# Optimization experiments

Hardware: AMD Instinct MI355X
Metric: run time of the kernel (lower is better)

The kernel has to match this reference:

```python
import jax, jax.numpy as jnp
import numpy as np

B, H, S, D = 4, 16, 2048, 64
SCALE = float(D ** 0.5)


def setup_inputs() -> dict:
    key = jax.random.key(0)
    kq, kk, kv = jax.random.split(key, 3)
    q = jax.random.normal(kq, (B, H, S, D), dtype=jnp.float32)
    k = jax.random.normal(kk, (B, H, S, D), dtype=jnp.float32)
    v = jax.random.normal(kv, (B, H, S, D), dtype=jnp.float32)
    return {"q": q, "k": k, "v": v}


def reference(q, k, v):
    # score: (B, H, S, S)
    score = jnp.einsum('bhqd,bhkd->bhqk', q, k) / SCALE
    seq_len = q.shape[-2]
    # causal mask: True above the diagonal (future positions) -> -inf
    mask = jnp.triu(jnp.ones((seq_len, seq_len), dtype=bool), k=1)
    score = jnp.where(mask, -jnp.inf, score)
    attn = jax.nn.softmax(score, axis=-1)
    return jnp.einsum('bhqk,bhkd->bhqd', attn, v)
```

## Files before the change

### kernel.cpp

```cpp
#include <hip/hip_runtime.h>
#include <math.h>

constexpr int S = 2048, D = 64;
constexpr int BH = 64;
constexpr int QTILE = 256;
constexpr int KVB = 64;
constexpr float QSCALE = 0.18033688011112042f;
constexpr float MBIAS = -8.0f;

typedef float f32x4 __attribute__((ext_vector_type(4)));
typedef float f32x16 __attribute__((ext_vector_type(16)));
typedef _Float16 f16x8 __attribute__((ext_vector_type(8)));
typedef unsigned int u32;
typedef unsigned int u32x2 __attribute__((ext_vector_type(2)));
typedef unsigned int u32x4 __attribute__((ext_vector_type(4)));

#define MFMA32(a, b, c) __builtin_amdgcn_mfma_f32_32x32x16_f16((a), (b), (c), 0, 0, 0)

#if __has_builtin(__builtin_amdgcn_exp2f)
#define EXP2(x) __builtin_amdgcn_exp2f(x)
#else
#define EXP2(x) exp2f(x)
#endif

__device__ __forceinline__ u32 pkbits(float a, float b) {
  return __builtin_bit_cast(u32, __builtin_amdgcn_cvt_pkrtz(a, b));
}
__device__ __forceinline__ void plswap(u32& a, u32& b) {
  asm volatile("v_permlane32_swap_b32 %0, %1" : "+v"(a), "+v"(b));
}
__device__ __forceinline__ int swzb(int row) { return ((row & 7) ^ (row >> 3)) << 3; }

#define BARRIER_LGKM()                                          \
  do {                                                          \
    asm volatile("s_waitcnt lgkmcnt(0)" ::: "memory");          \
    __builtin_amdgcn_s_barrier();                               \
    __builtin_amdgcn_sched_barrier(0);                          \
  } while (0)

__device__ __forceinline__ void qk_tile(
    const int ctmax, const int q32, const int hi,
    const _Float16* __restrict__ Kb, const f16x8 (&bq)[4],
    f32x16& st0, f32x16& st1) {
#pragma unroll
  for (int r = 0; r < 16; ++r) { st0[r] = MBIAS; st1[r] = MBIAS; }
  __builtin_amdgcn_s_setprio(1);
#pragma unroll
  for (int t = 0; t < 4; ++t) {
    f16x8 a = *(const f16x8*)&Kb[(q32 << 6) + (swzb(q32) ^ (16 * t + 8 * hi))];
    st0 = MFMA32(a, bq[t], st0);
  }
  if (ctmax) {
    const int row = 32 + q32;
#pragma unroll
    for (int t = 0; t < 4; ++t) {
      f16x8 a = *(const f16x8*)&Kb[(row << 6) + (swzb(row) ^ (16 * t + 8 * hi))];
      st1 = MFMA32(a, bq[t], st1);
    }
  }
  __builtin_amdgcn_s_setprio(0);
}

__device__ __forceinline__ void smpv_tile(
    const int rel, const int ctmax, const int q32, const int hi,
    const _Float16* __restrict__ Vb,
    f32x16& st0, f32x16& st1, f32x16& od0, f32x16& od1, float& l) {
  const bool needmask = (32 * ctmax + 31 > rel);
  if (needmask) {
    const int qrel = rel + q32;
#pragma unroll
    for (int gq = 0; gq < 4; ++gq)
#pragma unroll
      for (int i = 0; i < 4; ++i) {
        if (8 * gq + 4 * hi + i > qrel) st0[4 * gq + i] = -INFINITY;
        if (ctmax && (32 + 8 * gq + 4 * hi + i > qrel)) st1[4 * gq + i] = -INFINITY;
      }
  }

  float ps = 0.f;
#pragma unroll
  for (int r = 0; r < 16; ++r) { const float p = EXP2(st0[r]); st0[r] = p; ps += p; }
  if (ctmax)
#pragma unroll
    for (int r = 0; r < 16; ++r) { const float p = EXP2(st1[r]); st1[r] = p; ps += p; }
  l += ps;

  __builtin_amdgcn_s_setprio(1);
#define PV_CT(stv, CT)                                                          \
  _Pragma("unroll")                                                             \
  for (int t = 0; t < 2; ++t) {                                                 \
    u32 x0 = pkbits(stv[8 * t + 0], stv[8 * t + 1]);                            \
    u32 x1 = pkbits(stv[8 * t + 2], stv[8 * t + 3]);                            \
    u32 y0 = pkbits(stv[8 * t + 4], stv[8 * t + 5]);                            \
    u32 y1 = pkbits(stv[8 * t + 6], stv[8 * t + 7]);                            \
    plswap(x0, y0); plswap(x1, y1);                                             \
    const f16x8 pf = __builtin_bit_cast(f16x8, (u32x4){x0, x1, y0, y1});        \
    const int kcol = (2 * (CT) + t) * 16 + 8 * hi;                              \
    { const f16x8 vf = *(const f16x8*)&Vb[(q32 << 6) + (swzb(q32) ^ kcol)];     \
      od0 = MFMA32(vf, pf, od0); }                                              \
    { const int row = 32 + q32;                                                 \
      const f16x8 vf = *(const f16x8*)&Vb[(row << 6) + (swzb(row) ^ kcol)];     \
      od1 = MFMA32(vf, pf, od1); }                                              \
  }
  PV_CT(st0, 0);
  if (ctmax) { PV_CT(st1, 1); }
#undef PV_CT
  __builtin_amdgcn_s_setprio(0);
}

__global__ __launch_bounds__(512, 2)
void attn_fwd(const float* __restrict__ qp, const float* __restrict__ kp,
              const float* __restrict__ vp, float* __restrict__ op) {
  __shared__ _Float16 Kl[4][KVB * 64];
  __shared__ _Float16 Vt[4][64 * KVB];

  const int bh = blockIdx.x;
  const int pa = blockIdx.y;

  const int tid = threadIdx.x;
  const int wid = tid >> 6;
  const int lane = tid & 63;
  const int q32 = lane & 31;
  const int hi = lane >> 5;

  const size_t base = (size_t)bh * (S * D);

  const int rp = tid >> 4;
  const int cg = tid & 15;
  const int r0 = 2 * rp, r1 = 2 * rp + 1;
  const int c4 = cg * 4;
  const int kw0 = (r0 << 6) + (swzb(r0) ^ c4);
  const int kw1 = (r1 << 6) + (swzb(r1) ^ c4);
  const int vw0 = ((c4 + 0) << 6) + (swzb(c4 + 0) ^ r0);
  const int vw1 = ((c4 + 1) << 6) + (swzb(c4 + 1) ^ r0);
  const int vw2 = ((c4 + 2) << 6) + (swzb(c4 + 2) ^ r0);
  const int vw3 = ((c4 + 3) << 6) + (swzb(c4 + 3) ^ r0);

  const float* kbase = kp + base + (size_t)r0 * D + c4;
  const float* vbase = vp + base + (size_t)r0 * D + c4;

#define LOADT(kt, K0, K1, V0, V1)                                        \
  do {                                                                   \
    const float* kg_ = kbase + ((size_t)(kt) << 12);                     \
    const float* vg_ = vbase + ((size_t)(kt) << 12);                     \
    K0 = *(const f32x4*)kg_; K1 = *(const f32x4*)(kg_ + D);              \
    V0 = *(const f32x4*)vg_; V1 = *(const f32x4*)(vg_ + D);              \
  } while (0)

#define WRITET(buf, K0, K1, V0, V1)                                      \
  do {                                                                   \
    u32x2 kA_, kB_;                                                      \
    kA_[0] = pkbits(K0[0], K0[1]); kA_[1] = pkbits(K0[2], K0[3]);        \
    kB_[0] = pkbits(K1[0], K1[1]); kB_[1] = pkbits(K1[2], K1[3]);        \
    *(u32x2*)&Kl[buf][kw0] = kA_;                                        \
    *(u32x2*)&Kl[buf][kw1] = kB_;                                        \
    *(u32*)&Vt[buf][vw0] = pkbits(V0[0], V1[0]);                         \
    *(u32*)&Vt[buf][vw1] = pkbits(V0[1], V1[1]);                         \
    *(u32*)&Vt[buf][vw2] = pkbits(V0[2], V1[2]);                         \
    *(u32*)&Vt[buf][vw3] = pkbits(V0[3], V1[3]);                         \
  } while (0)

  f32x4 ka0, ka1, va0, va1, kb0, kb1, vb0, vb1;

  for (int ph = 0; ph < 2; ++ph) {
    const int qt = ph ? (7 - pa) : pa;
    const int Rp = qt * QTILE + wid * 32;
    const int NT = 4 * qt + 4;

    f16x8 bq[4];
    {
      const float* qg = qp + base + (size_t)(Rp + q32) * D + 8 * hi;
#pragma unroll
      for (int t = 0; t < 4; ++t) {
        f32x4 a = *(const f32x4*)(qg + 16 * t);
        f32x4 b = *(const f32x4*)(qg + 16 * t + 4);
#pragma unroll
        for (int j = 0; j < 4; ++j) bq[t][j] = (_Float16)(a[j] * QSCALE);
#pragma unroll
        for (int j = 0; j < 4; ++j) bq[t][4 + j] = (_Float16)(b[j] * QSCALE);
      }
    }

    f32x16 od0 = {}, od1 = {};
    float l = 0.f;

    LOADT(0, ka0, ka1, va0, va1);
    LOADT(1, kb0, kb1, vb0, vb1);

    for (int ktp = 0; ktp < NT; ktp += 2) {
      const int b0 = ktp & 2;
      WRITET(b0, ka0, ka1, va0, va1);
      WRITET(b0 + 1, kb0, kb1, vb0, vb1);
      if (ktp + 2 < NT) {
        LOADT(ktp + 2, ka0, ka1, va0, va1);
        LOADT(ktp + 3, kb0, kb1, vb0, vb1);
      }
      BARRIER_LGKM();

      const int ck0 = ktp * KVB, ck1 = ck0 + KVB;
      const bool go0 = (ck0 <= Rp + 31), go1 = (ck1 <= Rp + 31);
      const int rel0 = Rp - ck0, rel1 = Rp - ck1;
      const int ctm0 = (rel0 >= 32) ? 1 : 0, ctm1 = (rel1 >= 32) ? 1 : 0;
      f32x16 s00, s01, s10, s11;
      if (go0) qk_tile(ctm0, q32, hi, Kl[b0], bq, s00, s01);
      if (go1) qk_tile(ctm1, q32, hi, Kl[b0 + 1], bq, s10, s11);
      if (go0) smpv_tile(rel0, ctm0, q32, hi, Vt[b0], s00, s01, od0, od1, l);
      if (go1) smpv_tile(rel1, ctm1, q32, hi, Vt[b0 + 1], s10, s11, od0, od1, l);
    }

    const float lt = l + __shfl_xor(l, 32);
    const float inv = 1.f / lt;
    float* og = op + base + (size_t)(Rp + q32) * D + 4 * hi;
#pragma unroll
    for (int gq = 0; gq < 4; ++gq) {
      f32x4 w0, w1;
#pragma unroll
      for (int i = 0; i < 4; ++i) w0[i] = od0[4 * gq + i] * inv;
#pragma unroll
      for (int i = 0; i < 4; ++i) w1[i] = od1[4 * gq + i] * inv;
      *(f32x4*)(og + 8 * gq) = w0;
      *(f32x4*)(og + 32 + 8 * gq) = w1;
    }
  }
#undef LOADT
#undef WRITET
}

extern "C" void kernel_launch(void* const* d_in, const int* in_sizes, int n_in,
                              void* d_out, int out_size, void* d_ws, size_t ws_size,
                              hipStream_t stream) {
  const float* q = (const float*)d_in[0];
  const float* k = (const float*)d_in[1];
  const float* v = (const float*)d_in[2];
  float* out = (float*)d_out;
  dim3 grid(BH, 4);
  attn_fwd<<<grid, 512, 0, stream>>>(q, k, v, out);
}
```

Before: 65.19 us.

## Software-pipeline QK of next KV tile with softmax and PV of current tile

Splits the fused softmax+PV routine into a softmax/pack stage and a PV MFMA stage. The loop now computes the next tile's QK^T while the current tile's packed probabilities await PV, so MFMA work can overlap the exp/pack VALU work. It also reuses a single pair of score accumulators instead of four, which lowers register pressure. The cost is more complex control flow and a dependency order the compiler must schedule well.

New measurement: 60.28 us. 7.5% less time.

```diff
diff --git a/kernel.cpp b/kernel.cpp
--- a/kernel.cpp
+++ b/kernel.cpp
@@ -61,10 +61,9 @@
   __builtin_amdgcn_s_setprio(0);
 }
 
-__device__ __forceinline__ void smpv_tile(
+__device__ __forceinline__ void sm_pack(
     const int rel, const int ctmax, const int q32, const int hi,
-    const _Float16* __restrict__ Vb,
-    f32x16& st0, f32x16& st1, f32x16& od0, f32x16& od1, float& l) {
+    f32x16& st0, f32x16& st1, float& l, u32x4 (&pf)[4]) {
   const bool needmask = (32 * ctmax + 31 > rel);
   if (needmask) {
     const int qrel = rel + q32;
@@ -85,26 +84,51 @@
     for (int r = 0; r < 16; ++r) { const float p = EXP2(st1[r]); st1[r] = p; ps += p; }
   l += ps;
 
+#define PACK1(dst, stv, t)                                               \
+  do {                                                                   \
+    u32 x0 = pkbits(stv[8 * t + 0], stv[8 * t + 1]);                     \
+    u32 x1 = pkbits(stv[8 * t + 2], stv[8 * t + 3]);                     \
+    u32 y0 = pkbits(stv[8 * t + 4], stv[8 * t + 5]);                     \
+    u32 y1 = pkbits(stv[8 * t + 6], stv[8 * t + 7]);                     \
+    plswap(x0, y0); plswap(x1, y1);                                      \
+    dst = (u32x4){x0, x1, y0, y1};                                       \
+  } while (0)
+  PACK1(pf[0], st0, 0);
+  PACK1(pf[1], st0, 1);
+  if (ctmax) {
+    PACK1(pf[2], st1, 0);
+    PACK1(pf[3], st1, 1);
+  }
+#undef PACK1
+}
+
+__device__ __forceinline__ void pv_tile(
+    const int ctmax, const int q32, const int hi,
+    const _Float16* __restrict__ Vb, const u32x4 (&pf)[4],
+    f32x16& od0, f32x16& od1) {
+  const int rowv = 32 + q32;
+  const int sw0 = swzb(q32), sw1 = swzb(rowv);
   __builtin_amdgcn_s_setprio(1);
-#define PV_CT(stv, CT)                                                          \
-  _Pragma("unroll")                                                             \
-  for (int t = 0; t < 2; ++t) {                                                 \
-    u32 x0 = pkbits(stv[8 * t + 0], stv[8 * t + 1]);                            \
-    u32 x1 = pkbits(stv[8 * t + 2], stv[8 * t + 3]);                            \
-    u32 y0 = pkbits(stv[8 * t + 4], stv[8 * t + 5]);                            \
-    u32 y1 = pkbits(stv[8 * t + 6], stv[8 * t + 7]);                            \
-    plswap(x0, y0); plswap(x1, y1);                                             \
-    const f16x8 pf = __builtin_bit_cast(f16x8, (u32x4){x0, x1, y0, y1});        \
-    const int kcol = (2 * (CT) + t) * 16 + 8 * hi;                              \
-    { const f16x8 vf = *(const f16x8*)&Vb[(q32 << 6) + (swzb(q32) ^ kcol)];     \
-      od0 = MFMA32(vf, pf, od0); }                                              \
-    { const int row = 32 + q32;                                                 \
-      const f16x8 vf = *(const f16x8*)&Vb[(row << 6) + (swzb(row) ^ kcol)];     \
-      od1 = MFMA32(vf, pf, od1); }                                              \
-  }
-  PV_CT(st0, 0);
-  if (ctmax) { PV_CT(st1, 1); }
-#undef PV_CT
+#pragma unroll
+  for (int i = 0; i < 2; ++i) {
+    const f16x8 pfr = __builtin_bit_cast(f16x8, pf[i]);
+    const int kcol = i * 16 + 8 * hi;
+    const f16x8 vf0 = *(const f16x8*)&Vb[(q32 << 6) + (sw0 ^ kcol)];
+    const f16x8 vf1 = *(const f16x8*)&Vb[(rowv << 6) + (sw1 ^ kcol)];
+    od0 = MFMA32(vf0, pfr, od0);
+    od1 = MFMA32(vf1, pfr, od1);
+  }
+  if (ctmax) {
+#pragma unroll
+    for (int i = 0; i < 2; ++i) {
+      const f16x8 pfr = __builtin_bit_cast(f16x8, pf[2 + i]);
+      const int kcol = 32 + i * 16 + 8 * hi;
+      const f16x8 vf0 = *(const f16x8*)&Vb[(q32 << 6) + (sw0 ^ kcol)];
+      const f16x8 vf1 = *(const f16x8*)&Vb[(rowv << 6) + (sw1 ^ kcol)];
+      od0 = MFMA32(vf0, pfr, od0);
+      od1 = MFMA32(vf1, pfr, od1);
+    }
+  }
   __builtin_amdgcn_s_setprio(0);
 }
 
@@ -201,11 +225,20 @@
       const bool go0 = (ck0 <= Rp + 31), go1 = (ck1 <= Rp + 31);
       const int rel0 = Rp - ck0, rel1 = Rp - ck1;
       const int ctm0 = (rel0 >= 32) ? 1 : 0, ctm1 = (rel1 >= 32) ? 1 : 0;
-      f32x16 s00, s01, s10, s11;
-      if (go0) qk_tile(ctm0, q32, hi, Kl[b0], bq, s00, s01);
-      if (go1) qk_tile(ctm1, q32, hi, Kl[b0 + 1], bq, s10, s11);
-      if (go0) smpv_tile(rel0, ctm0, q32, hi, Vt[b0], s00, s01, od0, od1, l);
-      if (go1) smpv_tile(rel1, ctm1, q32, hi, Vt[b0 + 1], s10, s11, od0, od1, l);
+      f32x16 st0, st1;
+      u32x4 pf[4];
+      if (go1) {
+        qk_tile(ctm0, q32, hi, Kl[b0], bq, st0, st1);
+        sm_pack(rel0, ctm0, q32, hi, st0, st1, l, pf);
+        qk_tile(ctm1, q32, hi, Kl[b0 + 1], bq, st0, st1);
+        pv_tile(ctm0, q32, hi, Vt[b0], pf, od0, od1);
+        sm_pack(rel1, ctm1, q32, hi, st0, st1, l, pf);
+        pv_tile(ctm1, q32, hi, Vt[b0 + 1], pf, od0, od1);
+      } else if (go0) {
+        qk_tile(ctm0, q32, hi, Kl[b0], bq, st0, st1);
+        sm_pack(rel0, ctm0, q32, hi, st0, st1, l, pf);
+        pv_tile(ctm0, q32, hi, Vt[b0], pf, od0, od1);
+      }
     }
 
     const float lt = l + __shfl_xor(l, 32);
```
